# Performance work log

Hardware: AMD Instinct MI355X
Metric: run time of the kernel (lower is better)

## Reference

```python
import jax, jax.numpy as jnp
import numpy as np

B, N, F_IN, F_OUT, E = 8, 4096, 256, 256, 131072


def setup_inputs() -> dict:
    key = jax.random.key(0)
    kx, ke, kw = jax.random.split(key, 3)
    x = jax.random.normal(kx, (B, N, F_IN), dtype=jnp.float32)
    edge_index = jax.random.randint(ke, (2, E), 0, N, dtype=jnp.int32)
    # Xavier-uniform init for weight, zeros for bias (matches reset_parameters)
    limit = float(np.sqrt(6.0 / (F_IN + F_OUT)))
    weight = jax.random.uniform(kw, (F_IN, F_OUT), dtype=jnp.float32,
                                minval=-limit, maxval=limit)
    bias = jnp.zeros((F_OUT,), dtype=jnp.float32)
    return {"x": x, "edge_index": edge_index, "weight": weight, "bias": bias}


def reference(x, edge_index, weight, bias):
    # x: (B, N, F_in) -> transformed: (B, N, F_out)
    xt = jnp.einsum("bnf,fo->bno", x, weight)
    n_nodes = x.shape[1]
    # Adjacency is identical for every batch element in the original
    # (built from the same edge_index inside the loop) -> build once.
    # .set(1.0) matches torch's `adj[src, dst] = 1.0` (duplicates collapse).
    adj = jnp.zeros((n_nodes, n_nodes), dtype=xt.dtype)
    adj = adj.at[edge_index[0], edge_index[1]].set(1.0)
    degree = adj.sum(axis=1, keepdims=True) + 1e-6  # (N, 1)
    adj_norm = adj / degree
    # Aggregate: out[b] = adj_norm @ xt[b], batched as one einsum
    out = jnp.einsum("ij,bjf->bif", adj_norm, xt)
    return out + bias
```

## Files before the change

### kernel.cpp

```cpp
#include <hip/hip_runtime.h>
#include <hip/hip_bf16.h>


#define GC_B     8
#define GC_N     4096
#define GC_F     256
#define GC_E     131072
#define GC_M     (GC_B * GC_N)
#define MASK_WPR (GC_N / 32)

typedef __attribute__((ext_vector_type(8))) short         short8;
typedef __attribute__((ext_vector_type(4))) float         float4v;
typedef __attribute__((ext_vector_type(4))) unsigned int  uint4v;

static __device__ __forceinline__ unsigned short f2bf_rne(float f) {
    unsigned u = __builtin_bit_cast(unsigned, f);
    u += 0x7fffu + ((u >> 16) & 1u);
    return (unsigned short)(u >> 16);
}
static __device__ __forceinline__ float bflo(unsigned u) {
    return __builtin_bit_cast(float, u << 16);
}
static __device__ __forceinline__ float bfhi(unsigned u) {
    return __builtin_bit_cast(float, u & 0xffff0000u);
}

__global__ void build_mask_kernel(const int* __restrict__ ei,
                                  unsigned* __restrict__ mask) {
    int e = blockIdx.x * blockDim.x + threadIdx.x;
    if (e < GC_E) {
        int s = ei[e];
        int d = ei[GC_E + e];
        atomicOr(&mask[s * MASK_WPR + (d >> 5)], 1u << (d & 31));
    }
}

__global__ __launch_bounds__(128) void pack_mask_kernel(unsigned* __restrict__ mask) {
    __shared__ unsigned short list[256];
    __shared__ int cnt;
    const int i = blockIdx.x;
    const int t = threadIdx.x;

    if (t == 0) cnt = 0;
    unsigned w = mask[i * MASK_WPR + t];
    __syncthreads();

    const int base = t * 32;
    while (w) {
        const int b = __builtin_ctz(w);
        w &= w - 1;
        const int p = atomicAdd(&cnt, 1);
        if (p < 255) list[p + 1] = (unsigned short)(base + b);
    }
    __syncthreads();
    if (t == 0) list[0] = (unsigned short)(cnt < 255 ? cnt : 255);
    __syncthreads();

    ((unsigned*)(mask + i * MASK_WPR))[t] = ((const unsigned*)list)[t];
}

__global__ __launch_bounds__(256) void convert_x_kernel(
        const float* __restrict__ X, unsigned short* __restrict__ Xb) {
    const size_t i = ((size_t)blockIdx.x * 256 + threadIdx.x) * 8;
    const float4v v0 = *(const float4v*)(X + i);
    const float4v v1 = *(const float4v*)(X + i + 4);
    union { unsigned short h[8]; short8 s; } u;
    u.h[0] = f2bf_rne(v0[0]); u.h[1] = f2bf_rne(v0[1]);
    u.h[2] = f2bf_rne(v0[2]); u.h[3] = f2bf_rne(v0[3]);
    u.h[4] = f2bf_rne(v1[0]); u.h[5] = f2bf_rne(v1[1]);
    u.h[6] = f2bf_rne(v1[2]); u.h[7] = f2bf_rne(v1[3]);
    *(short8*)(Xb + i) = u.s;
}

__global__ __launch_bounds__(256) void aggregate_kernel(
        const unsigned short* __restrict__ Xb, const unsigned* __restrict__ mask,
        unsigned short* __restrict__ aggb) {
    __shared__ unsigned short list[256];
    __shared__ float part[8][32][9];

    const int bn = blockIdx.x;
    const int i  = bn & (GC_N - 1);
    const int b  = bn >> 12;
    const int t  = threadIdx.x;

    if (t < 32)
        ((uint4v*)list)[t] = ((const uint4v*)(mask + i * MASK_WPR))[t];
    __syncthreads();

    const int deg = list[0];
    const int fg  = t & 31;
    const int ks  = t >> 5;

    const unsigned short* xbase = Xb + (size_t)b * GC_N * GC_F + fg * 8;
    float accA[8] = {}, accB[8] = {};
    int k = ks;
    for (; k + 8 < deg; k += 16) {
        const uint4v v0 = *(const uint4v*)(xbase + (size_t)list[1 + k] * GC_F);
        const uint4v v1 = *(const uint4v*)(xbase + (size_t)list[9 + k] * GC_F);
        #pragma unroll
        for (int e = 0; e < 4; e++) {
            accA[2 * e]     += bflo(v0[e]);
            accA[2 * e + 1] += bfhi(v0[e]);
            accB[2 * e]     += bflo(v1[e]);
            accB[2 * e + 1] += bfhi(v1[e]);
        }
    }
    if (k < deg) {
        const uint4v v0 = *(const uint4v*)(xbase + (size_t)list[1 + k] * GC_F);
        #pragma unroll
        for (int e = 0; e < 4; e++) {
            accA[2 * e]     += bflo(v0[e]);
            accA[2 * e + 1] += bfhi(v0[e]);
        }
    }

    #pragma unroll
    for (int e = 0; e < 8; e++) part[ks][fg][e] = accA[e] + accB[e];
    __syncthreads();

    if (t < 32) {
        const float inv = 1.0f / ((float)deg + 1e-6f);
        uint4v o;
        #pragma unroll
        for (int e = 0; e < 4; e++) {
            float s0 = 0.f, s1 = 0.f;
            #pragma unroll
            for (int s = 0; s < 8; s++) {
                s0 += part[s][t][2 * e];
                s1 += part[s][t][2 * e + 1];
            }
            s0 *= inv; s1 *= inv;
            o[e] = (unsigned)f2bf_rne(s0) | ((unsigned)f2bf_rne(s1) << 16);
        }
        *(uint4v*)(aggb + (size_t)bn * GC_F + t * 8) = o;
    }
}

__global__ __launch_bounds__(256) void convert_w_kernel(
        const float* __restrict__ W, unsigned short* __restrict__ Wt) {
    const int n = blockIdx.x;
    const int k = threadIdx.x;
    Wt[n * GC_F + k] = f2bf_rne(W[k * GC_F + n]);
}

#define MROWS 128
__global__ __launch_bounds__(256) void gemm_bias_kernel(
        const unsigned short* __restrict__ Ab,
        const unsigned short* __restrict__ Wt,
        const float* __restrict__ bias, float* __restrict__ out) {
    const int n0   = blockIdx.y * 64;
    const int lane = threadIdx.x & 63;
    const int w    = threadIdx.x >> 6;
    const int r    = lane & 15;
    const int q    = lane >> 4;
    const int col  = n0 + 16 * w + r;

    const unsigned short* bp = Wt + (size_t)col * GC_F + q * 8;
    short8 bfr[8];
    #pragma unroll
    for (int kc = 0; kc < 8; kc++) bfr[kc] = *(const short8*)(bp + kc * 32);
    const float bv = bias[col];

    const int mbase = blockIdx.x * MROWS;
    #pragma unroll 2
    for (int mt = 0; mt < MROWS / 16; mt++) {
        const int m0 = mbase + mt * 16;
        const unsigned short* ap = Ab + (size_t)(m0 + r) * GC_F + q * 8;
        float4v acc = {0, 0, 0, 0};
        #pragma unroll
        for (int kc = 0; kc < 8; kc++)
            acc = __builtin_amdgcn_mfma_f32_16x16x32_bf16(
                *(const short8*)(ap + kc * 32), bfr[kc], acc, 0, 0, 0);
        #pragma unroll
        for (int rr = 0; rr < 4; rr++)
            out[(size_t)(m0 + 4 * q + rr) * GC_F + col] = acc[rr] + bv;
    }
}

extern "C" void kernel_launch(void* const* d_in, const int* in_sizes, int n_in,
                              void* d_out, int out_size, void* d_ws, size_t ws_size,
                              hipStream_t stream) {
    const float* x      = (const float*)d_in[0];
    const int*   ei     = (const int*)d_in[1];
    const float* weight = (const float*)d_in[2];
    const float* bias   = (const float*)d_in[3];
    float*       out    = (float*)d_out;

    unsigned short* aggb = (unsigned short*)d_ws;
    unsigned*       mask = (unsigned*)((char*)d_ws + (size_t)GC_M * GC_F * 2);
    unsigned short* Xb   = (unsigned short*)((char*)d_ws + (size_t)GC_M * GC_F * 2
                                             + (size_t)GC_N * MASK_WPR * 4);
    unsigned short* Wt   = Xb;

    hipMemsetAsync(mask, 0, (size_t)GC_N * MASK_WPR * sizeof(unsigned), stream);
    build_mask_kernel<<<(GC_E + 255) / 256, 256, 0, stream>>>(ei, mask);
    pack_mask_kernel<<<GC_N, 128, 0, stream>>>(mask);

    convert_x_kernel<<<(GC_M * GC_F) / 2048, 256, 0, stream>>>(x, Xb);

    aggregate_kernel<<<GC_M, 256, 0, stream>>>(Xb, mask, aggb);

    convert_w_kernel<<<GC_F, GC_F, 0, stream>>>(weight, Wt);

    dim3 ggrid(GC_M / MROWS, GC_F / 64);
    gemm_bias_kernel<<<ggrid, 256, 0, stream>>>(aggb, Wt, bias, out);
}
```

Baseline: 172.4 us.

## Assign one wavefront per aggregated row and vectorize GEMM output stores

```diff
diff --git a/kernel.cpp b/kernel.cpp
--- a/kernel.cpp
+++ b/kernel.cpp
@@ -75,28 +75,28 @@
 __global__ __launch_bounds__(256) void aggregate_kernel(
         const unsigned short* __restrict__ Xb, const unsigned* __restrict__ mask,
         unsigned short* __restrict__ aggb) {
-    __shared__ unsigned short list[256];
-    __shared__ float part[8][32][9];
-
-    const int bn = blockIdx.x;
-    const int i  = bn & (GC_N - 1);
-    const int b  = bn >> 12;
-    const int t  = threadIdx.x;
-
-    if (t < 32)
-        ((uint4v*)list)[t] = ((const uint4v*)(mask + i * MASK_WPR))[t];
-    __syncthreads();
-
-    const int deg = list[0];
-    const int fg  = t & 31;
-    const int ks  = t >> 5;
+    __shared__ unsigned short list[4][256];
+
+    const int w    = threadIdx.x >> 6;
+    const int lane = threadIdx.x & 63;
+    const int b    = blockIdx.x & 7;
+    const int i    = (blockIdx.x >> 3) * 4 + w;
+    const int bn   = b * GC_N + i;
+
+    if (lane < 32)
+        ((uint4v*)list[w])[lane] = ((const uint4v*)(mask + i * MASK_WPR))[lane];
+    __syncthreads();
+
+    const int deg = list[w][0];
+    const int fg  = lane & 31;
+    const int ks  = lane >> 5;
 
     const unsigned short* xbase = Xb + (size_t)b * GC_N * GC_F + fg * 8;
     float accA[8] = {}, accB[8] = {};
     int k = ks;
-    for (; k + 8 < deg; k += 16) {
-        const uint4v v0 = *(const uint4v*)(xbase + (size_t)list[1 + k] * GC_F);
-        const uint4v v1 = *(const uint4v*)(xbase + (size_t)list[9 + k] * GC_F);
+    for (; k + 2 < deg; k += 4) {
+        const uint4v v0 = *(const uint4v*)(xbase + (size_t)list[w][1 + k] * GC_F);
+        const uint4v v1 = *(const uint4v*)(xbase + (size_t)list[w][3 + k] * GC_F);
         #pragma unroll
         for (int e = 0; e < 4; e++) {
             accA[2 * e]     += bflo(v0[e]);
@@ -105,8 +105,8 @@
             accB[2 * e + 1] += bfhi(v1[e]);
         }
     }
-    if (k < deg) {
-        const uint4v v0 = *(const uint4v*)(xbase + (size_t)list[1 + k] * GC_F);
+    for (; k < deg; k += 2) {
+        const uint4v v0 = *(const uint4v*)(xbase + (size_t)list[w][1 + k] * GC_F);
         #pragma unroll
         for (int e = 0; e < 4; e++) {
             accA[2 * e]     += bflo(v0[e]);
@@ -114,25 +114,23 @@
         }
     }
 
+    float acc[8];
     #pragma unroll
-    for (int e = 0; e < 8; e++) part[ks][fg][e] = accA[e] + accB[e];
-    __syncthreads();
-
-    if (t < 32) {
+    for (int e = 0; e < 8; e++) {
+        acc[e] = accA[e] + accB[e];
+        acc[e] += __shfl_xor(acc[e], 32, 64);
+    }
+
+    if (ks == 0) {
         const float inv = 1.0f / ((float)deg + 1e-6f);
         uint4v o;
         #pragma unroll
         for (int e = 0; e < 4; e++) {
-            float s0 = 0.f, s1 = 0.f;
-            #pragma unroll
-            for (int s = 0; s < 8; s++) {
-                s0 += part[s][t][2 * e];
-                s1 += part[s][t][2 * e + 1];
-            }
-            s0 *= inv; s1 *= inv;
+            const float s0 = acc[2 * e] * inv;
+            const float s1 = acc[2 * e + 1] * inv;
             o[e] = (unsigned)f2bf_rne(s0) | ((unsigned)f2bf_rne(s1) << 16);
         }
-        *(uint4v*)(aggb + (size_t)bn * GC_F + t * 8) = o;
+        *(uint4v*)(aggb + (size_t)bn * GC_F + fg * 8) = o;
     }
 }
 
@@ -148,18 +146,16 @@
         const unsigned short* __restrict__ Ab,
         const unsigned short* __restrict__ Wt,
         const float* __restrict__ bias, float* __restrict__ out) {
-    const int n0   = blockIdx.y * 64;
     const int lane = threadIdx.x & 63;
-    const int w    = threadIdx.x >> 6;
     const int r    = lane & 15;
     const int q    = lane >> 4;
-    const int col  = n0 + 16 * w + r;
-
-    const unsigned short* bp = Wt + (size_t)col * GC_F + q * 8;
-    short8 bfr[8];
+    const int f0   = blockIdx.y * 64 + 16 * (threadIdx.x >> 6);
+
+    const unsigned short* wp = Wt + (size_t)(f0 + r) * GC_F + q * 8;
+    short8 wfr[8];
     #pragma unroll
-    for (int kc = 0; kc < 8; kc++) bfr[kc] = *(const short8*)(bp + kc * 32);
-    const float bv = bias[col];
+    for (int kc = 0; kc < 8; kc++) wfr[kc] = *(const short8*)(wp + kc * 32);
+    const float4v bv = *(const float4v*)(bias + f0 + 4 * q);
 
     const int mbase = blockIdx.x * MROWS;
     #pragma unroll 2
@@ -170,10 +166,8 @@
         #pragma unroll
         for (int kc = 0; kc < 8; kc++)
             acc = __builtin_amdgcn_mfma_f32_16x16x32_bf16(
-                *(const short8*)(ap + kc * 32), bfr[kc], acc, 0, 0, 0);
-        #pragma unroll
-        for (int rr = 0; rr < 4; rr++)
-            out[(size_t)(m0 + 4 * q + rr) * GC_F + col] = acc[rr] + bv;
+                wfr[kc], *(const short8*)(ap + kc * 32), acc, 0, 0, 0);
+        *(float4v*)(out + (size_t)(m0 + r) * GC_F + f0 + 4 * q) = acc + bv;
     }
 }
 
@@ -198,7 +192,7 @@
 
     convert_x_kernel<<<(GC_M * GC_F) / 2048, 256, 0, stream>>>(x, Xb);
 
-    aggregate_kernel<<<GC_M, 256, 0, stream>>>(Xb, mask, aggb);
+    aggregate_kernel<<<GC_M / 4, 256, 0, stream>>>(Xb, mask, aggb);
 
     convert_w_kernel<<<GC_F, GC_F, 0, stream>>>(weight, Wt);
 
```

Result: faster. 161.3 us (-6.4%).
